# Performance work log

Measured on AMD Instinct MI355X. Metric: run time of the kernel, lower is better.

Reference implementation:

```python
import jax, jax.numpy as jnp
import numpy as np

H = 512   # lstm_hidden_size
B = 64    # batch
S = 256   # seqlen


def setup_inputs() -> dict:
    key = jax.random.key(0)
    ks = jax.random.split(key, 6)
    scale = 1.0 / np.sqrt(H)  # PyTorch LSTM default init range
    return {
        "x": jax.random.normal(ks[0], (B, S, 2 * H), dtype=jnp.float32),
        "hi": jax.random.normal(ks[1], (B, S, 2 * H), dtype=jnp.float32),
        "W_ih": jax.random.uniform(ks[2], (4 * H, 5 * H), minval=-scale, maxval=scale, dtype=jnp.float32),
        "W_hh": jax.random.uniform(ks[3], (4 * H, H), minval=-scale, maxval=scale, dtype=jnp.float32),
        "b_ih": jax.random.uniform(ks[4], (4 * H,), minval=-scale, maxval=scale, dtype=jnp.float32),
        "b_hh": jax.random.uniform(ks[5], (4 * H,), minval=-scale, maxval=scale, dtype=jnp.float32),
    }


def _forward(x, hi, W_ih, W_hh, b_ih, b_hh):
    h_dim = W_hh.shape[1]
    bias = b_ih + b_hh
    xc = jnp.concatenate([x, hi], axis=-1)          # [B, S, 4H]
    xc = jnp.transpose(xc, (1, 0, 2))               # [S, B, 4H]
    batch = xc.shape[1]

    def cell(hc, inp_b):
        # inp_b: [5H]; PyTorch LSTM treats the batch dim as seq (batch_first=False quirk)
        h, c = hc
        gates = inp_b @ W_ih.T + h @ W_hh.T + bias  # [4H]
        i_g, f_g, g_g, o_g = jnp.split(gates, 4)
        i_g = jax.nn.sigmoid(i_g)
        f_g = jax.nn.sigmoid(f_g)
        g_g = jnp.tanh(g_g)
        o_g = jax.nn.sigmoid(o_g)
        c = f_g * c + i_g * g_g
        h = o_g * jnp.tanh(c)
        return (h, c), h

    def step(carry, x_i):
        out_prev, h, c = carry                      # out_prev: [B, H]
        inp = jnp.concatenate([x_i, out_prev], axis=-1)  # [B, 5H]
        (h, c), outs = jax.lax.scan(cell, (h, c), inp)    # scan over batch dim
        return (outs, h, c), outs

    init = (jnp.zeros((batch, h_dim), x.dtype),
            jnp.zeros((h_dim,), x.dtype),
            jnp.zeros((h_dim,), x.dtype))
    _, all_out = jax.lax.scan(step, init, xc)       # [S, B, H]
    return jnp.transpose(all_out, (1, 0, 2))        # [B, S, H]


def reference(x, hi, W_ih, W_hh, b_ih, b_hh):
    # Dropout layers are identity in eval mode.
    return _forward(x, hi, W_ih, W_hh, b_ih, b_hh)
```

## Files before the change

kernel.cpp:

```cpp
#include <hip/hip_runtime.h>

typedef _Float16 f16;
typedef _Float16 f16x2 __attribute__((ext_vector_type(2)));
typedef _Float16 f16x4 __attribute__((ext_vector_type(4)));
typedef _Float16 f16x8 __attribute__((ext_vector_type(8)));
typedef float f32x4 __attribute__((ext_vector_type(4)));
typedef unsigned int u32;
typedef unsigned int u32x4 __attribute__((ext_vector_type(4)));
typedef unsigned long long ull;

#define HD 512
#define T_TOT 16384
#define RING 128
#define NWG 32
#define NTH 512

static const size_t O_XC    = 0;
static const size_t O_W1    = 67108864;
static const size_t O_WHH   = 75497472;
static const size_t O_W2    = 77594624;
static const size_t O_G     = 79691776;
static const size_t O_PRING = 213909504;

__device__ __forceinline__ float dot2f(f16x2 a, f16x2 b, float c) {
#if __has_builtin(__builtin_amdgcn_fdot2)
    return __builtin_amdgcn_fdot2(a, b, c, false);
#else
    return fmaf((float)a[0], (float)b[0], fmaf((float)a[1], (float)b[1], c));
#endif
}
__device__ __forceinline__ f16x2 bcf(u32 u) { return __builtin_bit_cast(f16x2, u); }

__device__ __forceinline__ float sigf(float x) { return 1.0f / (1.0f + __expf(-x)); }
__device__ __forceinline__ float tanhfast(float x) { return 1.0f - 2.0f / (__expf(2.0f * x) + 1.0f); }

__device__ __forceinline__ ull ld_a64(const ull* p) {
    return __hip_atomic_load(p, __ATOMIC_RELAXED, __HIP_MEMORY_SCOPE_AGENT);
}
__device__ __forceinline__ void st_a64(ull* p, ull v) {
    __hip_atomic_store(p, v, __ATOMIC_RELAXED, __HIP_MEMORY_SCOPE_AGENT);
}

__global__ __launch_bounds__(256) void conv_xc(const float* __restrict__ x,
                                               const float* __restrict__ hi,
                                               f16* __restrict__ xc) {
    int gid = blockIdx.x * 256 + threadIdx.x;
    int t = gid >> 9;
    int k = (gid & 511) << 2;
    int b = t & 63, s = t >> 6;
    const float* src = (k < 1024) ? (x  + ((size_t)((b << 8) + s) << 10) + k)
                                  : (hi + ((size_t)((b << 8) + s) << 10) + (k - 1024));
    float4 v = *reinterpret_cast<const float4*>(src);
    f16x4 o = { (_Float16)v.x, (_Float16)v.y, (_Float16)v.z, (_Float16)v.w };
    *reinterpret_cast<f16x4*>(xc + ((size_t)t << 11) + k) = o;
}

__global__ __launch_bounds__(256) void conv_w1(const float* __restrict__ wih,
                                               f16* __restrict__ w1) {
    int gid = blockIdx.x * 256 + threadIdx.x;
    int j = gid >> 9;
    int k = (gid & 511) << 2;
    float4 v = *reinterpret_cast<const float4*>(wih + (size_t)j * 2560 + k);
    f16x4 o = { (_Float16)v.x, (_Float16)v.y, (_Float16)v.z, (_Float16)v.w };
    *reinterpret_cast<f16x4*>(w1 + ((size_t)j << 11) + k) = o;
}

__global__ __launch_bounds__(256) void conv_wc(const float* __restrict__ whh,
                                               const float* __restrict__ wih,
                                               f16* __restrict__ whhf,
                                               f16* __restrict__ w2f) {
    int gid = blockIdx.x * 256 + threadIdx.x;
    int j = gid >> 7;
    int k = (gid & 127) << 2;
    float4 a = *reinterpret_cast<const float4*>(whh + (size_t)j * 512 + k);
    f16x4 oa = { (_Float16)a.x, (_Float16)a.y, (_Float16)a.z, (_Float16)a.w };
    *reinterpret_cast<f16x4*>(whhf + ((size_t)j << 9) + k) = oa;
    float4 bv = *reinterpret_cast<const float4*>(wih + (size_t)j * 2560 + 2048 + k);
    f16x4 ob = { (_Float16)bv.x, (_Float16)bv.y, (_Float16)bv.z, (_Float16)bv.w };
    *reinterpret_cast<f16x4*>(w2f + ((size_t)j << 9) + k) = ob;
}

__global__ __launch_bounds__(256) void gemm_pre(const f16* __restrict__ XC,
                                                const f16* __restrict__ W1,
                                                const float* __restrict__ b_ih,
                                                const float* __restrict__ b_hh,
                                                float* __restrict__ G) {
    int w = threadIdx.x >> 6, l = threadIdx.x & 63;
    int R0 = blockIdx.y * 128 + (w >> 1) * 64;
    int C0 = blockIdx.x * 128 + (w & 1) * 64;
    int lr = l & 15, kb = l >> 4;
    f32x4 acc[4][4] = {};
    const f16* Abase = XC + (size_t)(R0 + lr) * 2048 + kb * 8;
    const f16* Bbase = W1 + (size_t)(C0 + lr) * 2048 + kb * 8;
    for (int kk = 0; kk < 2048; kk += 32) {
        f16x8 av[4], bv[4];
#pragma unroll
        for (int i = 0; i < 4; i++)
            av[i] = *reinterpret_cast<const f16x8*>(Abase + (size_t)(i * 16) * 2048 + kk);
#pragma unroll
        for (int i = 0; i < 4; i++)
            bv[i] = *reinterpret_cast<const f16x8*>(Bbase + (size_t)(i * 16) * 2048 + kk);
#pragma unroll
        for (int fr = 0; fr < 4; fr++)
#pragma unroll
            for (int fc = 0; fc < 4; fc++)
                acc[fr][fc] = __builtin_amdgcn_mfma_f32_16x16x32_f16(av[fr], bv[fc], acc[fr][fc], 0, 0, 0);
    }
#pragma unroll
    for (int fc = 0; fc < 4; fc++) {
        int col = C0 + fc * 16 + lr;
        float bias = b_ih[col] + b_hh[col];
#pragma unroll
        for (int fr = 0; fr < 4; fr++) {
#pragma unroll
            for (int r = 0; r < 4; r++) {
                int row = R0 + fr * 16 + kb * 4 + r;
                G[(size_t)row * 2048 + col] = acc[fr][fc][r] + bias;
            }
        }
    }
}

__global__ __launch_bounds__(NTH, 1) void lstm_chain(const float* __restrict__ G,
                                                     const f16* __restrict__ Whhf,
                                                     const f16* __restrict__ W2f,
                                                     ull* __restrict__ ring,
                                                     float* __restrict__ out) {
    const int wg = blockIdx.x;
    const int tid = threadIdx.x;
    const int wv = tid >> 6, l = tid & 63;
    const int g = wv & 3, uh = wv >> 2;
    const int rr = ((l & 1) << 2) | (l & 2) | ((l >> 2) & 1);
    const int row0 = g * 512 + wg * 16 + uh * 8;
    const int growD = row0 + rr;

    __shared__ u32 hist[64][256];
    __shared__ __align__(16) float part[2][16][4];

    for (int i = tid; i < 4096; i += NTH)
        reinterpret_cast<u32x4*>(hist)[i] = (u32x4){0u, 0u, 0u, 0u};

    u32x4 w1v[8], w2v[8];
    {
        const f16* p1a = Whhf + (size_t)row0 * 512 + 8 * l;
        const f16* p1b = p1a + 2048;
        const f16* p2a = W2f + (size_t)row0 * 512 + 8 * l;
        const f16* p2b = p2a + 2048;
        asm volatile(
            "global_load_dwordx4 %0, %16, off\n\t"
            "global_load_dwordx4 %1, %16, off offset:1024\n\t"
            "global_load_dwordx4 %2, %16, off offset:2048\n\t"
            "global_load_dwordx4 %3, %16, off offset:3072\n\t"
            "global_load_dwordx4 %4, %17, off\n\t"
            "global_load_dwordx4 %5, %17, off offset:1024\n\t"
            "global_load_dwordx4 %6, %17, off offset:2048\n\t"
            "global_load_dwordx4 %7, %17, off offset:3072\n\t"
            "global_load_dwordx4 %8, %18, off\n\t"
            "global_load_dwordx4 %9, %18, off offset:1024\n\t"
            "global_load_dwordx4 %10, %18, off offset:2048\n\t"
            "global_load_dwordx4 %11, %18, off offset:3072\n\t"
            "global_load_dwordx4 %12, %19, off\n\t"
            "global_load_dwordx4 %13, %19, off offset:1024\n\t"
            "global_load_dwordx4 %14, %19, off offset:2048\n\t"
            "global_load_dwordx4 %15, %19, off offset:3072\n\t"
            "s_waitcnt vmcnt(0)"
            : "=&v"(w1v[0]), "=&v"(w1v[1]), "=&v"(w1v[2]), "=&v"(w1v[3]),
              "=&v"(w1v[4]), "=&v"(w1v[5]), "=&v"(w1v[6]), "=&v"(w1v[7]),
              "=&v"(w2v[0]), "=&v"(w2v[1]), "=&v"(w2v[2]), "=&v"(w2v[3]),
              "=&v"(w2v[4]), "=&v"(w2v[5]), "=&v"(w2v[6]), "=&v"(w2v[7])
            : "v"(p1a), "v"(p1b), "v"(p2a), "v"(p2b)
            : "memory");
    }

    float cst = 0.0f;
    float gv = (l < 8) ? G[growD] : 0.0f;
    __syncthreads();

    for (int t = 0; t < T_TOT; t++) {
        const int buf = t & 1;

        u32x4 hv = *reinterpret_cast<const u32x4*>(&hist[t & 63][4 * l]);
        float ac[8] = {0.f, 0.f, 0.f, 0.f, 0.f, 0.f, 0.f, 0.f};
        {
            f16x2 h0 = bcf(hv.x), h1 = bcf(hv.y), h2 = bcf(hv.z), h3 = bcf(hv.w);
#pragma unroll
            for (int r = 0; r < 8; r++) {
                ac[r] = dot2f(bcf(w2v[r].x), h0, ac[r]);
                ac[r] = dot2f(bcf(w2v[r].y), h1, ac[r]);
                ac[r] = dot2f(bcf(w2v[r].z), h2, ac[r]);
                ac[r] = dot2f(bcf(w2v[r].w), h3, ac[r]);
            }
        }

        const ull* pB = ring + (size_t)((t - 1) & (RING - 1)) * 256 + 4 * l;
        const u32 want = (u32)t;
        ull b0 = ld_a64(pB + 0), b1 = ld_a64(pB + 1);
        ull b2 = ld_a64(pB + 2), b3 = ld_a64(pB + 3);
        while ((((u32)(b0 >> 32) ^ want) | ((u32)(b1 >> 32) ^ want) |
                ((u32)(b2 >> 32) ^ want) | ((u32)(b3 >> 32) ^ want)) != 0u) {
            b0 = ld_a64(pB + 0); b1 = ld_a64(pB + 1);
            b2 = ld_a64(pB + 2); b3 = ld_a64(pB + 3);
        }

        int tn = (t + 1 < T_TOT) ? t + 1 : t;
        float gnext = (l < 8) ? G[(size_t)tn * 2048 + growD] : 0.0f;

        if (wv == 0)
            *reinterpret_cast<u32x4*>(&hist[(t - 1) & 63][4 * l]) =
                (u32x4){(u32)b0, (u32)b1, (u32)b2, (u32)b3};

        {
            f16x2 h0 = bcf((u32)b0), h1 = bcf((u32)b1), h2 = bcf((u32)b2), h3 = bcf((u32)b3);
#pragma unroll
            for (int r = 0; r < 8; r++) {
                ac[r] = dot2f(bcf(w1v[r].x), h0, ac[r]);
                ac[r] = dot2f(bcf(w1v[r].y), h1, ac[r]);
                ac[r] = dot2f(bcf(w1v[r].z), h2, ac[r]);
                ac[r] = dot2f(bcf(w1v[r].w), h3, ac[r]);
            }
        }

        const bool s0 = l & 1, s1 = l & 2, s2 = l & 4;
        float b4_0 = (s0 ? ac[4] : ac[0]) + __shfl_xor((s0 ? ac[0] : ac[4]), 1);
        float b4_1 = (s0 ? ac[5] : ac[1]) + __shfl_xor((s0 ? ac[1] : ac[5]), 1);
        float b4_2 = (s0 ? ac[6] : ac[2]) + __shfl_xor((s0 ? ac[2] : ac[6]), 1);
        float b4_3 = (s0 ? ac[7] : ac[3]) + __shfl_xor((s0 ? ac[3] : ac[7]), 1);
        float c2_0 = (s1 ? b4_2 : b4_0) + __shfl_xor((s1 ? b4_0 : b4_2), 2);
        float c2_1 = (s1 ? b4_3 : b4_1) + __shfl_xor((s1 ? b4_1 : b4_3), 2);
        float d    = (s2 ? c2_1 : c2_0) + __shfl_xor((s2 ? c2_0 : c2_1), 4);
        d += __shfl_xor(d, 8);
        d += __shfl_xor(d, 16);
        d += __shfl_xor(d, 32);
        if (l < 8)
            part[buf][uh * 8 + rr][g] = d + gv;
        gv = gnext;
        __syncthreads();

        const int u = l & 15;
        float4 pg = *reinterpret_cast<const float4*>(part[buf][u]);
        float fi = sigf(pg.x), ff = sigf(pg.y);
        float fgg = tanhfast(pg.z), fo = sigf(pg.w);
        cst = ff * cst + fi * fgg;
        float h = fo * tanhfast(cst);

        u32 hb = (u32)__builtin_bit_cast(unsigned short, (f16)h);
        u32 plo = (u32)__shfl((int)hb, 2 * (l & 7));
        u32 phi = (u32)__shfl((int)hb, 2 * (l & 7) + 1);
        ull pv = (ull)(plo & 0xffffu) | ((ull)(phi & 0xffffu) << 16) |
                 ((ull)(u32)(t + 1) << 32);
        if (wv == 0 && l < 8)
            st_a64(ring + (size_t)(t & (RING - 1)) * 256 + wg * 8 + l, pv);
        if (wv == 1 && l < 16) {
            int b = t & 63, s = t >> 6;
            out[((size_t)((b << 8) + s)) * 512 + wg * 16 + l] = h;
        }
    }
}

extern "C" void kernel_launch(void* const* d_in, const int* in_sizes, int n_in,
                              void* d_out, int out_size, void* d_ws, size_t ws_size,
                              hipStream_t stream) {
    const float* x    = (const float*)d_in[0];
    const float* hi   = (const float*)d_in[1];
    const float* W_ih = (const float*)d_in[2];
    const float* W_hh = (const float*)d_in[3];
    const float* b_ih = (const float*)d_in[4];
    const float* b_hh = (const float*)d_in[5];

    char* ws = (char*)d_ws;
    f16*   XCf   = (f16*)(ws + O_XC);
    f16*   W1f   = (f16*)(ws + O_W1);
    f16*   Whhf  = (f16*)(ws + O_WHH);
    f16*   W2f   = (f16*)(ws + O_W2);
    float* G     = (float*)(ws + O_G);
    ull*   ring  = (ull*)(ws + O_PRING);

    hipMemsetAsync(ring, 0, (size_t)RING * 256 * sizeof(ull), stream);

    conv_xc<<<32768, 256, 0, stream>>>(x, hi, XCf);
    conv_w1<<<4096, 256, 0, stream>>>(W_ih, W1f);
    conv_wc<<<1024, 256, 0, stream>>>(W_hh, W_ih, Whhf, W2f);
    gemm_pre<<<dim3(16, 128), 256, 0, stream>>>(XCf, W1f, b_ih, b_hh, G);
    lstm_chain<<<NWG, NTH, 0, stream>>>(G, Whhf, W2f, ring, (float*)d_out);
}
```

Measured before the change: 30.30 ms.

## Co-locate recurrent chain workgroups on one XCD with L2-scoped ring exchange

Launches 256 cooperative workgroups and has each read its XCC_ID and elect a slot, so that all 32 active workgroups sit on the same XCD and the rest exit. The per-step hidden-state exchange then uses sc0 loads and stores on a local ring that stay in the shared L2, with a bounded retry before falling back to an agent-scope global ring, which is also written every step. The goal is lower cross-workgroup handoff latency in the serial 16384-step recurrence. It adds an election protocol, a duplicated store per step, and relies on cooperative launch residency, falling back to the old launch if that fails.

New measurement: 37.63 ms. 24.2% more time.

```diff
diff --git a/kernel.cpp b/kernel.cpp
--- a/kernel.cpp
+++ b/kernel.cpp
@@ -20,7 +20,9 @@
 static const size_t O_WHH   = 75497472;
 static const size_t O_W2    = 77594624;
 static const size_t O_G     = 79691776;
-static const size_t O_PRING = 213909504;
+static const size_t O_RINGL = 213909504;
+static const size_t O_RINGG = 214171648;
+static const size_t O_ELECT = 214433792;
 
 __device__ __forceinline__ float dot2f(f16x2 a, f16x2 b, float c) {
 #if __has_builtin(__builtin_amdgcn_fdot2)
@@ -39,6 +41,17 @@
 }
 __device__ __forceinline__ void st_a64(ull* p, ull v) {
     __hip_atomic_store(p, v, __ATOMIC_RELAXED, __HIP_MEMORY_SCOPE_AGENT);
+}
+__device__ __forceinline__ void ld4_sc0(const ull* p, ull& a, ull& b, ull& c, ull& d) {
+    asm volatile("global_load_dwordx2 %0, %4, off sc0\n\t"
+                 "global_load_dwordx2 %1, %4, off offset:8 sc0\n\t"
+                 "global_load_dwordx2 %2, %4, off offset:16 sc0\n\t"
+                 "global_load_dwordx2 %3, %4, off offset:24 sc0\n\t"
+                 "s_waitcnt vmcnt(0)"
+                 : "=&v"(a), "=&v"(b), "=&v"(c), "=&v"(d) : "v"(p) : "memory");
+}
+__device__ __forceinline__ void st1_sc0(ull* p, ull v) {
+    asm volatile("global_store_dwordx2 %0, %1, off sc0" :: "v"(p), "v"(v) : "memory");
 }
 
 __global__ __launch_bounds__(256) void conv_xc(const float* __restrict__ x,
@@ -121,21 +134,45 @@
     }
 }
 
-__global__ __launch_bounds__(NTH, 1) void lstm_chain(const float* __restrict__ G,
-                                                     const f16* __restrict__ Whhf,
-                                                     const f16* __restrict__ W2f,
-                                                     ull* __restrict__ ring,
-                                                     float* __restrict__ out) {
-    const int wg = blockIdx.x;
+template <int COOP>
+__global__ __launch_bounds__(NTH, 1) void lstm_chain_t(const float* __restrict__ G,
+                                                       const f16* __restrict__ Whhf,
+                                                       const f16* __restrict__ W2f,
+                                                       ull* __restrict__ ringL,
+                                                       ull* __restrict__ ringG,
+                                                       int* __restrict__ elect,
+                                                       float* __restrict__ out) {
+    __shared__ u32 hist[64][256];
+    __shared__ __align__(16) float part[2][16][4];
+    __shared__ int s_slot;
+
     const int tid = threadIdx.x;
+    int wg;
+    if (COOP) {
+        if (tid == 0) {
+            int xcc = 0;
+            asm volatile("s_getreg_b32 %0, hwreg(HW_REG_XCC_ID, 0, 32)" : "=s"(xcc));
+            xcc &= 7;
+            int s = atomicAdd(&elect[xcc], 1);
+            if (s == 31) atomicCAS(&elect[8], 0, xcc + 1);
+            int w;
+            do {
+                w = __hip_atomic_load(&elect[8], __ATOMIC_RELAXED, __HIP_MEMORY_SCOPE_AGENT);
+            } while (w == 0);
+            s_slot = (w - 1 == xcc && s < 32) ? s : -1;
+        }
+        __syncthreads();
+        wg = s_slot;
+        if (wg < 0) return;
+    } else {
+        wg = blockIdx.x;
+    }
+
     const int wv = tid >> 6, l = tid & 63;
     const int g = wv & 3, uh = wv >> 2;
     const int rr = ((l & 1) << 2) | (l & 2) | ((l >> 2) & 1);
     const int row0 = g * 512 + wg * 16 + uh * 8;
     const int growD = row0 + rr;
-
-    __shared__ u32 hist[64][256];
-    __shared__ __align__(16) float part[2][16][4];
 
     for (int i = tid; i < 4096; i += NTH)
         reinterpret_cast<u32x4*>(hist)[i] = (u32x4){0u, 0u, 0u, 0u};
@@ -174,6 +211,7 @@
 
     float cst = 0.0f;
     float gv = (l < 8) ? G[growD] : 0.0f;
+    bool fb = false;
     __syncthreads();
 
     for (int t = 0; t < T_TOT; t++) {
@@ -192,14 +230,25 @@
             }
         }
 
-        const ull* pB = ring + (size_t)((t - 1) & (RING - 1)) * 256 + 4 * l;
+        const size_t soff = (size_t)((t - 1) & (RING - 1)) * 256 + 4 * l;
         const u32 want = (u32)t;
-        ull b0 = ld_a64(pB + 0), b1 = ld_a64(pB + 1);
-        ull b2 = ld_a64(pB + 2), b3 = ld_a64(pB + 3);
-        while ((((u32)(b0 >> 32) ^ want) | ((u32)(b1 >> 32) ^ want) |
-                ((u32)(b2 >> 32) ^ want) | ((u32)(b3 >> 32) ^ want)) != 0u) {
-            b0 = ld_a64(pB + 0); b1 = ld_a64(pB + 1);
-            b2 = ld_a64(pB + 2); b3 = ld_a64(pB + 3);
+        ull b0, b1, b2, b3;
+        bool got = false;
+        if (COOP && !fb) {
+            for (int tries = 0; tries < 256 && !got; ++tries) {
+                ld4_sc0(ringL + soff, b0, b1, b2, b3);
+                got = ((((u32)(b0 >> 32) ^ want) | ((u32)(b1 >> 32) ^ want) |
+                        ((u32)(b2 >> 32) ^ want) | ((u32)(b3 >> 32) ^ want)) == 0u);
+            }
+            if (!got) fb = true;
+        }
+        if (!got) {
+            const ull* pG = ringG + soff;
+            do {
+                b0 = ld_a64(pG + 0); b1 = ld_a64(pG + 1);
+                b2 = ld_a64(pG + 2); b3 = ld_a64(pG + 3);
+            } while ((((u32)(b0 >> 32) ^ want) | ((u32)(b1 >> 32) ^ want) |
+                      ((u32)(b2 >> 32) ^ want) | ((u32)(b3 >> 32) ^ want)) != 0u);
         }
 
         int tn = (t + 1 < T_TOT) ? t + 1 : t;
@@ -248,8 +297,13 @@
         u32 phi = (u32)__shfl((int)hb, 2 * (l & 7) + 1);
         ull pv = (ull)(plo & 0xffffu) | ((ull)(phi & 0xffffu) << 16) |
                  ((ull)(u32)(t + 1) << 32);
-        if (wv == 0 && l < 8)
-            st_a64(ring + (size_t)(t & (RING - 1)) * 256 + wg * 8 + l, pv);
+        const size_t woff = (size_t)(t & (RING - 1)) * 256 + wg * 8 + l;
+        if (COOP) {
+            if (wv == 0 && l < 8) st1_sc0(ringL + woff, pv);
+            if (wv == 2 && l < 8) st_a64(ringG + woff, pv);
+        } else {
+            if (wv == 0 && l < 8) st_a64(ringG + woff, pv);
+        }
         if (wv == 1 && l < 16) {
             int b = t & 63, s = t >> 6;
             out[((size_t)((b << 8) + s)) * 512 + wg * 16 + l] = h;
@@ -273,13 +327,26 @@
     f16*   Whhf  = (f16*)(ws + O_WHH);
     f16*   W2f   = (f16*)(ws + O_W2);
     float* G     = (float*)(ws + O_G);
-    ull*   ring  = (ull*)(ws + O_PRING);
-
-    hipMemsetAsync(ring, 0, (size_t)RING * 256 * sizeof(ull), stream);
+    ull*   ringL = (ull*)(ws + O_RINGL);
+    ull*   ringG = (ull*)(ws + O_RINGG);
+    int*   elect = (int*)(ws + O_ELECT);
+    float* outp  = (float*)d_out;
+
+    hipMemsetAsync(ringL, 0, 2 * (size_t)RING * 256 * sizeof(ull) + 64, stream);
 
     conv_xc<<<32768, 256, 0, stream>>>(x, hi, XCf);
     conv_w1<<<4096, 256, 0, stream>>>(W_ih, W1f);
     conv_wc<<<1024, 256, 0, stream>>>(W_hh, W_ih, Whhf, W2f);
     gemm_pre<<<dim3(16, 128), 256, 0, stream>>>(XCf, W1f, b_ih, b_hh, G);
-    lstm_chain<<<NWG, NTH, 0, stream>>>(G, Whhf, W2f, ring, (float*)d_out);
-}
+
+    const f16* cWhhf = Whhf;
+    const f16* cW2f  = W2f;
+    const float* cG  = G;
+    void* kargs[] = { (void*)&cG, (void*)&cWhhf, (void*)&cW2f,
+                      (void*)&ringL, (void*)&ringG, (void*)&elect, (void*)&outp };
+    hipError_t e = hipLaunchCooperativeKernel((const void*)lstm_chain_t<1>,
+                                              dim3(256), dim3(NTH), kargs, 0, stream);
+    if (e != hipSuccess) {
+        lstm_chain_t<0><<<NWG, NTH, 0, stream>>>(G, Whhf, W2f, ringL, ringG, elect, outp);
+    }
+}
```
